# Performance work log

Measured on AMD Instinct MI355X. Metric: run time of the kernel, lower is better.

The kernel has to match this reference:

```python
import jax, jax.numpy as jnp
import numpy as np


def setup_inputs() -> dict:
    key = jax.random.key(0)
    k1, k2 = jax.random.split(key)
    query = jax.random.normal(k1, (16, 256, 32, 32), dtype=jnp.float32)
    search_map = jax.random.normal(k2, (16, 256, 64, 64), dtype=jnp.float32)
    return {"query": query, "search_map": search_map}


def reference(query, search_map):
    # query: [bs, c, h, w]; search_map: [bs, c, H, W]
    bs, c, h, w = query.shape
    # pad H and W by h//2, w//2 on each side (matches F.pad(left,right,top,bottom))
    padded = jnp.pad(search_map, ((0, 0), (0, 0), (h // 2, h // 2), (w // 2, w // 2)))

    def corr_one(map_, q_):
        # map_: [c, Hp, Wp], q_: [c, h, w]
        # per-sample cross-correlation: the query acts as a single-output conv kernel
        out = jax.lax.conv_general_dilated(
            map_[None],            # [1, c, Hp, Wp]
            q_[None],              # [1, c, h, w] -> OIHW
            window_strides=(1, 1),
            padding="VALID",
            dimension_numbers=("NCHW", "OIHW", "NCHW"),
        )
        return out[0]              # [1, Hout, Wout]

    # vmap over the batch: each sample uses its own query as the kernel
    return jax.vmap(corr_one)(padded, query)  # [bs, 1, Hout, Wout]
```

## Files before the change

kernel.cpp:

```cpp
#include <hip/hip_runtime.h>
#include <stdint.h>

typedef __bf16 bf16x8 __attribute__((ext_vector_type(8)));
typedef float  f32x4  __attribute__((ext_vector_type(4)));
typedef uint32_t u32x4 __attribute__((ext_vector_type(4)));

__device__ __forceinline__ uint16_t f2bf(float f) {
    uint32_t u = __builtin_bit_cast(uint32_t, f);
    u += 0x7FFFu + ((u >> 16) & 1u);
    return (uint16_t)(u >> 16);
}

__global__ __launch_bounds__(256) void qtrans_kernel(const float* __restrict__ Q,
                                                     uint16_t* __restrict__ Qt,
                                                     float* __restrict__ out) {
    __shared__ float T[8 * 1064];
    const int ch = blockIdx.x, b = blockIdx.y;
    const int tid = threadIdx.x;

    {
        int g = (b * 32 + ch) * 256 + tid;
        if (g < 67600) out[g] = 0.f;
    }

    const float* src = Q + ((size_t)(b * 256 + ch * 8)) * 1024;
    #pragma unroll
    for (int it = 0; it < 32; ++it) {
        int r = tid + it * 256;
        int c8 = r >> 10, rem = r & 1023;
        T[c8 * 1064 + (rem >> 5) * 33 + (rem & 31)] = src[(size_t)c8 * 1024 + rem];
    }
    __syncthreads();

    uint32_t* dst = (uint32_t*)Qt;
    #pragma unroll
    for (int it = 0; it < 16; ++it) {
        int o2 = tid + it * 256;
        int t  = (o2 & 3) * 2;
        int il = (o2 >> 2) & 15;
        int j  = (o2 >> 6) & 31;
        int ih = (o2 >> 11) & 1;
        float v0 = T[t * 1064 + (ih * 16 + il) * 33 + j];
        float v1 = T[(t + 1) * 1064 + (ih * 16 + il) * 33 + j];
        uint32_t pk = (uint32_t)f2bf(v0) | ((uint32_t)f2bf(v1) << 16);
        size_t oi = ((((size_t)(b * 2 + ih) * 32 + j) * 32 + ch) * 16 + il) * 4 + (t >> 1);
        dst[oi] = pk;
    }
}

__global__ __launch_bounds__(256, 4) void corr_kernel(const float* __restrict__ S,
                                                      const uint16_t* __restrict__ Qt,
                                                      float* __restrict__ out) {
    __shared__ __align__(16) char smem[40960];
    uint16_t* S_l = (uint16_t*)smem;
    float*    Pw  = (float*)smem;

    const int bid = blockIdx.x;
    const int b = bid & 15, d = bid >> 4;
    const int tid = threadIdx.x, wave = tid >> 6, lane = tid & 63;
    const int l15 = lane & 15, l4 = lane >> 4;

    {
        const u32x4 z = {};
        for (int zi = tid; zi < 512; zi += 256) {
            int ch = zi >> 4, r = zi & 15;
            *(u32x4*)&S_l[ch * 640 + r * 8] = z;
        }
    }
    {
        const int sx = tid & 63, w = tid >> 6;
        const float* sp = S + ((size_t)b * 256) * 4096 + (size_t)d * 64;
        #pragma unroll
        for (int k = 0; k < 8; ++k) {
            int ch = w * 8 + k;
            float v[8];
            #pragma unroll
            for (int cc = 0; cc < 8; ++cc)
                v[cc] = sp[(size_t)(ch * 8 + cc) * 4096 + sx];
            u32x4 pk;
            #pragma unroll
            for (int q = 0; q < 4; ++q)
                pk[q] = (uint32_t)f2bf(v[2 * q]) | ((uint32_t)f2bf(v[2 * q + 1]) << 16);
            *(u32x4*)&S_l[ch * 640 + (sx + 16) * 8] = pk;
        }
    }

    const uint16_t* Bb = Qt + (size_t)b * 262144 + l4 * 128 + l15 * 8;

    bf16x8 C0, C1, C2, C3;
    {
        const int s0 = (2 * wave) & 7;
        const uint16_t* p0 = Bb + wave * 4096 + s0 * 512;
        C0 = *(const bf16x8*)(p0);
        C1 = *(const bf16x8*)(p0 + 131072);
        C2 = *(const bf16x8*)(p0 + 65536);
        C3 = *(const bf16x8*)(p0 + 196608);
    }

    __syncthreads();

    f32x4 acc[5][2] = {};

    #pragma unroll
    for (int n = 0; n < 32; ++n) {
        const int jj = n >> 3;
        const int s  = ((n & 7) + 2 * wave) & 7;
        const int j0a = wave + jj * 4;

        const int nn = (n < 31) ? (n + 1) : 31;
        const int jn = nn >> 3;
        const int sn = ((nn & 7) + 2 * wave) & 7;
        const uint16_t* pn = Bb + (wave + jn * 4) * 4096 + sn * 512;
        bf16x8 N0 = *(const bf16x8*)(pn);
        bf16x8 N1 = *(const bf16x8*)(pn + 131072);
        bf16x8 N2 = *(const bf16x8*)(pn + 65536);
        bf16x8 N3 = *(const bf16x8*)(pn + 196608);

        const int chb = (s * 4 + l4) * 640;
        bf16x8 A[5];
        #pragma unroll
        for (int t = 0; t < 5; ++t) {
            int rr = j0a + t * 16 + l15;
            rr = (rr < 80) ? rr : 0;
            A[t] = *(const bf16x8*)&S_l[chb + rr * 8];
        }
        __builtin_amdgcn_sched_barrier(0);

        __builtin_amdgcn_s_setprio(1);
        #pragma unroll
        for (int t = 0; t < 5; ++t) {
            acc[t][0] = __builtin_amdgcn_mfma_f32_16x16x32_bf16(A[t], C0, acc[t][0], 0, 0, 0);
            acc[t][1] = __builtin_amdgcn_mfma_f32_16x16x32_bf16(A[t], C1, acc[t][1], 0, 0, 0);
        }
        #pragma unroll
        for (int t = 1; t < 5; ++t) {
            acc[t - 1][0] = __builtin_amdgcn_mfma_f32_16x16x32_bf16(A[t], C2, acc[t - 1][0], 0, 0, 0);
            acc[t - 1][1] = __builtin_amdgcn_mfma_f32_16x16x32_bf16(A[t], C3, acc[t - 1][1], 0, 0, 0);
        }
        __builtin_amdgcn_s_setprio(0);

        C0 = N0; C1 = N1; C2 = N2; C3 = N3;
    }

    __syncthreads();
    {
        float* pw = Pw + wave * 2560;
        #pragma unroll
        for (int m = 0; m < 5; ++m)
            #pragma unroll
            for (int n = 0; n < 2; ++n) {
                const int row = n * 16 + l15;
                const int grp = m * 4 + (l4 ^ (l15 & 3));
                *(f32x4*)&pw[row * 80 + grp * 4] = acc[m][n];
            }
    }
    __syncthreads();
    for (int e = tid; e < 65 * 32; e += 256) {
        int x = e % 65, i = e / 65;
        int y = d - i + 16;
        if ((unsigned)y < 65u) {
            const int gx = ((((x >> 2) ^ (i & 3)) << 2) | (x & 3));
            const int o  = i * 80 + gx;
            float v = Pw[0 * 2560 + o] + Pw[1 * 2560 + o]
                    + Pw[2 * 2560 + o] + Pw[3 * 2560 + o];
            atomicAdd(out + ((size_t)b * 4225 + (size_t)y * 65 + x), v);
        }
    }
}

__global__ __launch_bounds__(256) void naive_kernel(const float* __restrict__ Q,
                                                    const float* __restrict__ S,
                                                    float* __restrict__ out) {
    int gid = blockIdx.x * 256 + threadIdx.x;
    if (gid >= 67600) return;
    int b = gid / 4225, r = gid % 4225, y = r / 65, x = r % 65;
    int jlo = 16 - x; if (jlo < 0) jlo = 0;
    int jhi = 80 - x; if (jhi > 32) jhi = 32;
    float acc = 0.f;
    for (int c = 0; c < 256; ++c) {
        const float* Sb = S + ((size_t)(b * 256 + c)) * 4096;
        const float* Qb = Q + ((size_t)(b * 256 + c)) * 1024;
        for (int i = 0; i < 32; ++i) {
            int dd = y + i - 16;
            if ((unsigned)dd >= 64u) continue;
            const float* Sr = Sb + dd * 64 + (x - 16);
            const float* Qr = Qb + i * 32;
            for (int j = jlo; j < jhi; ++j) acc += Sr[j] * Qr[j];
        }
    }
    out[gid] = acc;
}

extern "C" void kernel_launch(void* const* d_in, const int* in_sizes, int n_in,
                              void* d_out, int out_size, void* d_ws, size_t ws_size,
                              hipStream_t stream) {
    (void)in_sizes; (void)n_in; (void)out_size;
    const float* Q = (const float*)d_in[0];
    const float* S = (const float*)d_in[1];
    float* out = (float*)d_out;

    const size_t QT_BYTES = (size_t)16 * 2 * 32 * 32 * 16 * 8 * 2;

    if (ws_size < QT_BYTES) {
        naive_kernel<<<(67600 + 255) / 256, 256, 0, stream>>>(Q, S, out);
        return;
    }
    uint16_t* Qt = (uint16_t*)d_ws;

    qtrans_kernel<<<dim3(32, 16), 256, 0, stream>>>(Q, Qt, out);
    corr_kernel<<<1024, 256, 0, stream>>>(S, Qt, out);
}
```

Before: 130.9 us.

## Fuse query transpose and correlation into one cooperative kernel with grid sync

Merges the query transpose/bf16 conversion kernel and the correlation kernel into a single cooperative launch. Each of the 1024 blocks transposes a slice of Q into the workspace, stages its search tile, then waits at a grid-wide barrier before the MFMA loop. This removes one kernel launch and lets the search-map load overlap with the transpose. In exchange it adds grid-sync cost, and it needs all 1024 blocks to be co-resident, falling back to two launches if the cooperative launch fails.

Measured after the change: 271.4 us. 2.07x slower.

```diff
diff --git a/kernel.cpp b/kernel.cpp
--- a/kernel.cpp
+++ b/kernel.cpp
@@ -1,5 +1,8 @@
 #include <hip/hip_runtime.h>
+#include <hip/hip_cooperative_groups.h>
 #include <stdint.h>
+
+namespace cg = cooperative_groups;
 
 typedef __bf16 bf16x8 __attribute__((ext_vector_type(8)));
 typedef float  f32x4  __attribute__((ext_vector_type(4)));
@@ -9,6 +12,159 @@
     uint32_t u = __builtin_bit_cast(uint32_t, f);
     u += 0x7FFFu + ((u >> 16) & 1u);
     return (uint16_t)(u >> 16);
+}
+
+__global__ __launch_bounds__(256, 4) void fused_kernel(const float* __restrict__ Q,
+                                                       const float* __restrict__ S,
+                                                       uint16_t* __restrict__ Qt,
+                                                       float* __restrict__ out) {
+    __shared__ __align__(16) char smem[40960];
+    const int bid = blockIdx.x;
+    const int b = bid & 15, d = bid >> 4;
+    const int tid = threadIdx.x, wave = tid >> 6, lane = tid & 63;
+    const int l15 = lane & 15, l4 = lane >> 4;
+
+    { int g = bid * 256 + tid; if (g < 67600) out[g] = 0.f; }
+
+    {
+        float* T = (float*)smem;
+        const int ch = d >> 1, jh = d & 1;
+        const float* src = Q + ((size_t)(b * 256 + ch * 8)) * 1024;
+        #pragma unroll
+        for (int it = 0; it < 16; ++it) {
+            int r = tid + it * 256;
+            int c8 = r >> 9, rem = r & 511;
+            int i = rem >> 4, jl = rem & 15;
+            T[c8 * 545 + i * 17 + jl] = src[(size_t)c8 * 1024 + i * 32 + jh * 16 + jl];
+        }
+        __syncthreads();
+        uint32_t* dst = (uint32_t*)Qt;
+        #pragma unroll
+        for (int it = 0; it < 8; ++it) {
+            int o2 = tid + it * 256;
+            int p  = o2 & 3;
+            int il = (o2 >> 2) & 15;
+            int jl = (o2 >> 6) & 15;
+            int ih = (o2 >> 10) & 1;
+            float v0 = T[(2 * p) * 545 + (ih * 16 + il) * 17 + jl];
+            float v1 = T[(2 * p + 1) * 545 + (ih * 16 + il) * 17 + jl];
+            uint32_t pk = (uint32_t)f2bf(v0) | ((uint32_t)f2bf(v1) << 16);
+            int j = jh * 16 + jl;
+            size_t oi = ((((size_t)(b * 2 + ih) * 32 + j) * 32 + ch) * 16 + il) * 4 + p;
+            dst[oi] = pk;
+        }
+        __syncthreads();
+    }
+
+    uint16_t* S_l = (uint16_t*)smem;
+    float*    Pw  = (float*)smem;
+
+    {
+        const u32x4 z = {};
+        for (int zi = tid; zi < 512; zi += 256) {
+            int ch = zi >> 4, r = zi & 15;
+            *(u32x4*)&S_l[ch * 640 + r * 8] = z;
+        }
+    }
+    {
+        const int sx = tid & 63, w = tid >> 6;
+        const float* sp = S + ((size_t)b * 256) * 4096 + (size_t)d * 64;
+        #pragma unroll
+        for (int k = 0; k < 8; ++k) {
+            int ch = w * 8 + k;
+            float v[8];
+            #pragma unroll
+            for (int cc = 0; cc < 8; ++cc)
+                v[cc] = sp[(size_t)(ch * 8 + cc) * 4096 + sx];
+            u32x4 pk;
+            #pragma unroll
+            for (int q = 0; q < 4; ++q)
+                pk[q] = (uint32_t)f2bf(v[2 * q]) | ((uint32_t)f2bf(v[2 * q + 1]) << 16);
+            *(u32x4*)&S_l[ch * 640 + (sx + 16) * 8] = pk;
+        }
+    }
+
+    cg::this_grid().sync();
+
+    const uint16_t* Bb = Qt + (size_t)b * 262144 + l4 * 128 + l15 * 8;
+
+    bf16x8 C0, C1, C2, C3;
+    {
+        const int s0 = (2 * wave) & 7;
+        const uint16_t* p0 = Bb + wave * 4096 + s0 * 512;
+        C0 = *(const bf16x8*)(p0);
+        C1 = *(const bf16x8*)(p0 + 131072);
+        C2 = *(const bf16x8*)(p0 + 65536);
+        C3 = *(const bf16x8*)(p0 + 196608);
+    }
+
+    f32x4 acc[5][2] = {};
+
+    #pragma unroll
+    for (int n = 0; n < 32; ++n) {
+        const int jj = n >> 3;
+        const int s  = ((n & 7) + 2 * wave) & 7;
+        const int j0a = wave + jj * 4;
+
+        const int nn = (n < 31) ? (n + 1) : 31;
+        const int jn = nn >> 3;
+        const int sn = ((nn & 7) + 2 * wave) & 7;
+        const uint16_t* pn = Bb + (wave + jn * 4) * 4096 + sn * 512;
+        bf16x8 N0 = *(const bf16x8*)(pn);
+        bf16x8 N1 = *(const bf16x8*)(pn + 131072);
+        bf16x8 N2 = *(const bf16x8*)(pn + 65536);
+        bf16x8 N3 = *(const bf16x8*)(pn + 196608);
+
+        const int chb = (s * 4 + l4) * 640;
+        bf16x8 A[5];
+        #pragma unroll
+        for (int t = 0; t < 5; ++t) {
+            int rr = j0a + t * 16 + l15;
+            rr = (rr < 80) ? rr : 0;
+            A[t] = *(const bf16x8*)&S_l[chb + rr * 8];
+        }
+        __builtin_amdgcn_sched_barrier(0);
+
+        __builtin_amdgcn_s_setprio(1);
+        #pragma unroll
+        for (int t = 0; t < 5; ++t) {
+            acc[t][0] = __builtin_amdgcn_mfma_f32_16x16x32_bf16(A[t], C0, acc[t][0], 0, 0, 0);
+            acc[t][1] = __builtin_amdgcn_mfma_f32_16x16x32_bf16(A[t], C1, acc[t][1], 0, 0, 0);
+        }
+        #pragma unroll
+        for (int t = 1; t < 5; ++t) {
+            acc[t - 1][0] = __builtin_amdgcn_mfma_f32_16x16x32_bf16(A[t], C2, acc[t - 1][0], 0, 0, 0);
+            acc[t - 1][1] = __builtin_amdgcn_mfma_f32_16x16x32_bf16(A[t], C3, acc[t - 1][1], 0, 0, 0);
+        }
+        __builtin_amdgcn_s_setprio(0);
+
+        C0 = N0; C1 = N1; C2 = N2; C3 = N3;
+    }
+
+    __syncthreads();
+    {
+        float* pw = Pw + wave * 2560;
+        #pragma unroll
+        for (int m = 0; m < 5; ++m)
+            #pragma unroll
+            for (int n = 0; n < 2; ++n) {
+                const int row = n * 16 + l15;
+                const int grp = m * 4 + (l4 ^ (l15 & 3));
+                *(f32x4*)&pw[row * 80 + grp * 4] = acc[m][n];
+            }
+    }
+    __syncthreads();
+    for (int e = tid; e < 65 * 32; e += 256) {
+        int x = e % 65, i = e / 65;
+        int y = d - i + 16;
+        if ((unsigned)y < 65u) {
+            const int gx = ((((x >> 2) ^ (i & 3)) << 2) | (x & 3));
+            const int o  = i * 80 + gx;
+            float v = Pw[0 * 2560 + o] + Pw[1 * 2560 + o]
+                    + Pw[2 * 2560 + o] + Pw[3 * 2560 + o];
+            atomicAdd(out + ((size_t)b * 4225 + (size_t)y * 65 + x), v);
+        }
+    }
 }
 
 __global__ __launch_bounds__(256) void qtrans_kernel(const float* __restrict__ Q,
@@ -17,12 +173,10 @@
     __shared__ float T[8 * 1064];
     const int ch = blockIdx.x, b = blockIdx.y;
     const int tid = threadIdx.x;
-
     {
         int g = (b * 32 + ch) * 256 + tid;
         if (g < 67600) out[g] = 0.f;
     }
-
     const float* src = Q + ((size_t)(b * 256 + ch * 8)) * 1024;
     #pragma unroll
     for (int it = 0; it < 32; ++it) {
@@ -31,7 +185,6 @@
         T[c8 * 1064 + (rem >> 5) * 33 + (rem & 31)] = src[(size_t)c8 * 1024 + rem];
     }
     __syncthreads();
-
     uint32_t* dst = (uint32_t*)Qt;
     #pragma unroll
     for (int it = 0; it < 16; ++it) {
@@ -86,7 +239,6 @@
     }
 
     const uint16_t* Bb = Qt + (size_t)b * 262144 + l4 * 128 + l15 * 8;
-
     bf16x8 C0, C1, C2, C3;
     {
         const int s0 = (2 * wave) & 7;
@@ -96,17 +248,14 @@
         C2 = *(const bf16x8*)(p0 + 65536);
         C3 = *(const bf16x8*)(p0 + 196608);
     }
-
     __syncthreads();
 
     f32x4 acc[5][2] = {};
-
     #pragma unroll
     for (int n = 0; n < 32; ++n) {
         const int jj = n >> 3;
         const int s  = ((n & 7) + 2 * wave) & 7;
         const int j0a = wave + jj * 4;
-
         const int nn = (n < 31) ? (n + 1) : 31;
         const int jn = nn >> 3;
         const int sn = ((nn & 7) + 2 * wave) & 7;
@@ -207,6 +356,12 @@
     }
     uint16_t* Qt = (uint16_t*)d_ws;
 
-    qtrans_kernel<<<dim3(32, 16), 256, 0, stream>>>(Q, Qt, out);
-    corr_kernel<<<1024, 256, 0, stream>>>(S, Qt, out);
-}
+    void* kargs[] = {(void*)&Q, (void*)&S, (void*)&Qt, (void*)&out};
+    hipError_t err = hipLaunchCooperativeKernel((const void*)fused_kernel,
+                                                dim3(1024), dim3(256),
+                                                kargs, 0, stream);
+    if (err != hipSuccess) {
+        qtrans_kernel<<<dim3(32, 16), 256, 0, stream>>>(Q, Qt, out);
+        corr_kernel<<<1024, 256, 0, stream>>>(S, Qt, out);
+    }
+}
```
